# Performance work log

Hardware: AMD Instinct MI355X
Metric: run time of the kernel (lower is better)

Reference implementation:

```python
import jax, jax.numpy as jnp
import numpy as np

N, D, DIN, B, M = 1280000, 128, 2048, 256, 4096
TAU, GAMMA = 0.07, 0.5

def _l2norm(x):
    # F.normalize(p=2, dim=1, eps=1e-12): x / max(||x||, eps)
    n = jnp.sqrt(jnp.sum(x * x, axis=-1, keepdims=True))
    return x / jnp.maximum(n, 1e-12)

def setup_inputs() -> dict:
    key = jax.random.key(0)
    k0, k1, k2, k3, k4, k5 = jax.random.split(key, 6)
    memory_bank = _l2norm(jax.random.normal(k0, (N, D), dtype=jnp.float32))
    outputs = jax.random.normal(k1, (B, DIN), dtype=jnp.float32)
    W = jax.random.normal(k2, (D, DIN), dtype=jnp.float32) * 0.02  # Linear weight (out,in)
    b = jnp.zeros((D,), dtype=jnp.float32)
    indices = jax.random.randint(k3, (B,), 0, N, dtype=jnp.int32)
    random_idxs = jax.random.randint(k4, (B, M), 0, N, dtype=jnp.int32)
    return {"outputs": outputs, "W": W, "b": b, "memory_bank": memory_bank,
            "indices": indices, "random_idxs": random_idxs}

def reference(outputs, W, b, memory_bank, indices, random_idxs):
    batch = outputs.shape[0]
    emb = _l2norm(outputs @ W.T + b)                     # (B, D)
    mb = jax.lax.stop_gradient(memory_bank)              # gathers happen under no_grad
    pos_mem = mb[indices]                                # (B, D) gather
    neg_mem = mb[random_idxs]                            # (B, M, D) gather
    pos = jnp.sum(emb * pos_mem, axis=-1) / TAU          # (B,)
    neg = jnp.einsum('bd,bmd->bm', emb, neg_mem) / TAU   # (B, M)
    # dynamic mode
    log_C_hat = jax.nn.logsumexp(neg, axis=1)            # (B,)
    log_data_prob = pos - jnp.logaddexp(pos, log_C_hat)  # (B,)
    log_noise_prob = log_C_hat[:, None] - jnp.logaddexp(neg, log_C_hat[:, None])  # (B, M)
    data_loss = -jnp.sum(log_data_prob) / batch
    noise_loss = -jnp.sum(log_noise_prob) / batch
    loss = data_loss + noise_loss
    # EMA memory-bank update entries (detached)
    entries = _l2norm(GAMMA * pos_mem + (1.0 - GAMMA) * emb)
    return (loss,
            jax.lax.stop_gradient(entries),
            jax.lax.stop_gradient(data_loss),
            jax.lax.stop_gradient(noise_loss))
```

## Files before the change

### kernel.cpp

```cpp
#include <hip/hip_runtime.h>
#include <math.h>

#define NB 1280000
#define D 128
#define DIN 2048
#define BB 256
#define MM 4096

constexpr float INV_TAU = 1.0f / 0.07f;
constexpr float GAMMA = 0.5f;

__device__ __forceinline__ float softplus_f(float x) {
    return x > 20.0f ? x : log1pf(expf(x));
}

__global__ __launch_bounds__(256) void emb_kernel(
    const float* __restrict__ outputs, const float* __restrict__ W,
    const float* __restrict__ bias, const float* __restrict__ mb,
    const int* __restrict__ indices,
    float* __restrict__ emb, float* __restrict__ pos,
    float* __restrict__ entries)
{
    __shared__ float4 xs4[DIN / 4];
    __shared__ float zbuf[D];
    __shared__ float red[256];
    const int b = blockIdx.x;
    const int t = threadIdx.x;
    const int wave = t >> 6, lane = t & 63;

    const float4* out4 = (const float4*)(outputs + (size_t)b * DIN);
    xs4[t]       = out4[t];
    xs4[t + 256] = out4[t + 256];
    __syncthreads();

    const float4* W4 = (const float4*)W;
    for (int i = 0; i < 32; ++i) {
        int d = i * 4 + wave;
        const float4* wrow = W4 + (size_t)d * (DIN / 4);
        float acc = 0.0f;
        #pragma unroll
        for (int r = 0; r < 8; ++r) {
            float4 wv = wrow[r * 64 + lane];
            float4 xv = xs4[r * 64 + lane];
            acc += wv.x * xv.x + wv.y * xv.y + wv.z * xv.z + wv.w * xv.w;
        }
        #pragma unroll
        for (int s = 32; s > 0; s >>= 1) acc += __shfl_xor(acc, s);
        if (lane == 0) zbuf[d] = acc + bias[d];
    }
    __syncthreads();

    float z = (t < D) ? zbuf[t] : 0.0f;
    red[t] = z * z;
    __syncthreads();
    for (int s = 128; s > 0; s >>= 1) { if (t < s) red[t] += red[t + s]; __syncthreads(); }
    float inv = 1.0f / fmaxf(sqrtf(red[0]), 1e-12f);
    __syncthreads();
    float e = z * inv;
    if (t < D) emb[(size_t)b * D + t] = e;

    int pidx = indices[b];
    float pm = (t < D) ? mb[(size_t)pidx * D + t] : 0.0f;
    red[t] = e * pm;
    __syncthreads();
    for (int s = 128; s > 0; s >>= 1) { if (t < s) red[t] += red[t + s]; __syncthreads(); }
    if (t == 0) pos[b] = red[0] * INV_TAU;
    __syncthreads();

    float en = GAMMA * pm + (1.0f - GAMMA) * e;
    red[t] = en * en;
    __syncthreads();
    for (int s = 128; s > 0; s >>= 1) { if (t < s) red[t] += red[t + s]; __syncthreads(); }
    float inv2 = 1.0f / fmaxf(sqrtf(red[0]), 1e-12f);
    if (t < D) entries[(size_t)b * D + t] = en * inv2;
}

__global__ __launch_bounds__(256) void neg_kernel(
    const float* __restrict__ mb, const int* __restrict__ ridx,
    const float* __restrict__ emb, float* __restrict__ neg,
    float* __restrict__ chunk_max, float* __restrict__ chunk_sum)
{
    __shared__ int idxs[512];
    __shared__ float gmax[8], gsum[8];
    const int blk = blockIdx.x;
    const int b = blk >> 3, c = blk & 7;
    const int m0 = c << 9;
    const int t = threadIdx.x;
    const int g = t >> 5, gl = t & 31;

    idxs[t]       = ridx[(size_t)b * MM + m0 + t];
    idxs[t + 256] = ridx[(size_t)b * MM + m0 + t + 256];
    const float4* emb4 = (const float4*)(emb + (size_t)b * D);
    float4 e4 = emb4[gl];
    __syncthreads();

    const float4* mb4 = (const float4*)mb;
    float* negrow = neg + (size_t)b * MM + m0;
    float mx = -INFINITY, sm = 0.0f;

    for (int it = 0; it < 32; ++it) {
        int r0 = it * 16 + g * 2;
        int i0 = idxs[r0], i1 = idxs[r0 + 1];
        float4 v0 = mb4[(size_t)i0 * 32 + gl];
        float4 v1 = mb4[(size_t)i1 * 32 + gl];
        float p0 = v0.x * e4.x + v0.y * e4.y + v0.z * e4.z + v0.w * e4.w;
        float p1 = v1.x * e4.x + v1.y * e4.y + v1.z * e4.z + v1.w * e4.w;
        #pragma unroll
        for (int s = 16; s > 0; s >>= 1) {
            p0 += __shfl_xor(p0, s);
            p1 += __shfl_xor(p1, s);
        }
        p0 *= INV_TAU; p1 *= INV_TAU;
        if (gl == 0) {
            negrow[r0] = p0; negrow[r0 + 1] = p1;
            float hi = fmaxf(p0, p1), lo = fminf(p0, p1);
            float pairsum = 1.0f + expf(lo - hi);
            if (hi > mx) { sm = sm * expf(mx - hi) + pairsum; mx = hi; }
            else         { sm += pairsum * expf(hi - mx); }
        }
    }
    if (gl == 0) { gmax[g] = mx; gsum[g] = sm; }
    __syncthreads();
    if (t == 0) {
        float Mx = gmax[0];
        for (int i = 1; i < 8; ++i) Mx = fmaxf(Mx, gmax[i]);
        float S = 0.0f;
        for (int i = 0; i < 8; ++i) S += gsum[i] * expf(gmax[i] - Mx);
        chunk_max[blk] = Mx;
        chunk_sum[blk] = S;
    }
}

__global__ __launch_bounds__(256) void logc_kernel(
    const float* __restrict__ chunk_max, const float* __restrict__ chunk_sum,
    const float* __restrict__ pos, float* __restrict__ logC,
    float* __restrict__ data_sum, float* __restrict__ noise_sum)
{
    __shared__ float red[256];
    const int t = threadIdx.x;
    float Mx = -INFINITY;
    for (int i = 0; i < 8; ++i) Mx = fmaxf(Mx, chunk_max[t * 8 + i]);
    float S = 0.0f;
    for (int i = 0; i < 8; ++i) S += chunk_sum[t * 8 + i] * expf(chunk_max[t * 8 + i] - Mx);
    float lc = Mx + logf(S);
    logC[t] = lc;
    red[t] = softplus_f(lc - pos[t]);
    __syncthreads();
    for (int s = 128; s > 0; s >>= 1) { if (t < s) red[t] += red[t + s]; __syncthreads(); }
    if (t == 0) { data_sum[0] = red[0]; noise_sum[0] = 0.0f; }
}

__global__ __launch_bounds__(256) void noise_kernel(
    const float* __restrict__ neg, const float* __restrict__ logC,
    float* __restrict__ noise_sum)
{
    __shared__ float red[256];
    const int t = threadIdx.x;
    size_t i = (size_t)blockIdx.x * 256 + t;
    int b = (int)(i >> 10);
    float lc = logC[b];
    float4 v = ((const float4*)neg)[i];
    float s = softplus_f(v.x - lc) + softplus_f(v.y - lc) +
              softplus_f(v.z - lc) + softplus_f(v.w - lc);
    red[t] = s;
    __syncthreads();
    for (int st = 128; st > 0; st >>= 1) { if (t < st) red[t] += red[t + st]; __syncthreads(); }
    if (t == 0) atomicAdd(noise_sum, red[0]);
}

__global__ void final_kernel(const float* __restrict__ data_sum,
                             const float* __restrict__ noise_sum,
                             float* __restrict__ out)
{
    float dl = data_sum[0] / (float)BB;
    float nl = noise_sum[0] / (float)BB;
    out[0] = dl + nl;
    out[1 + BB * D] = dl;
    out[2 + BB * D] = nl;
}

extern "C" void kernel_launch(void* const* d_in, const int* in_sizes, int n_in,
                              void* d_out, int out_size, void* d_ws, size_t ws_size,
                              hipStream_t stream) {
    const float* outputs = (const float*)d_in[0];
    const float* W       = (const float*)d_in[1];
    const float* bias    = (const float*)d_in[2];
    const float* mb      = (const float*)d_in[3];
    const int*   indices = (const int*)d_in[4];
    const int*   ridx    = (const int*)d_in[5];

    float* out = (float*)d_out;
    float* ws  = (float*)d_ws;

    float* emb       = ws;
    float* pos       = emb + BB * D;
    float* chunk_max = pos + BB;
    float* chunk_sum = chunk_max + BB * 8;
    float* logC      = chunk_sum + BB * 8;
    float* data_sum  = logC + BB;
    float* noise_sum = data_sum + 1;
    float* neg       = ws + 37380;

    float* entries = out + 1;

    emb_kernel<<<BB, 256, 0, stream>>>(outputs, W, bias, mb, indices, emb, pos, entries);
    neg_kernel<<<BB * 8, 256, 0, stream>>>(mb, ridx, emb, neg, chunk_max, chunk_sum);
    logc_kernel<<<1, 256, 0, stream>>>(chunk_max, chunk_sum, pos, logC, data_sum, noise_sum);
    noise_kernel<<<BB * MM / 4 / 256, 256, 0, stream>>>(neg, logC, noise_sum);
    final_kernel<<<1, 1, 0, stream>>>(data_sum, noise_sum, out);
}
```

Baseline: 867.7 us.

## Batch eight gathered rows per group and parallelize chunk logsumexp in neg_kernel

Each 32-lane group now issues eight independent memory-bank row gathers before reducing, instead of two per iteration. This raises memory-level parallelism on the random gather. Dot products are staged in shared memory, so the stores to neg become coalesced block-wide writes. The serial per-lane online softmax is replaced by block-wide max and sum reductions. Costs are more registers per thread and extra shared memory and barriers.

```diff
diff --git a/kernel.cpp b/kernel.cpp
--- a/kernel.cpp
+++ b/kernel.cpp
@@ -81,53 +81,59 @@
     float* __restrict__ chunk_max, float* __restrict__ chunk_sum)
 {
     __shared__ int idxs[512];
-    __shared__ float gmax[8], gsum[8];
+    __shared__ float pvals[512];
+    __shared__ float wm[4], wsum[4];
     const int blk = blockIdx.x;
     const int b = blk >> 3, c = blk & 7;
     const int m0 = c << 9;
     const int t = threadIdx.x;
     const int g = t >> 5, gl = t & 31;
+    const int wave = t >> 6, lane = t & 63;
 
     idxs[t]       = ridx[(size_t)b * MM + m0 + t];
-    idxs[t + 256] = ridx[(size_t)b * MM + m0 + t + 256];
-    const float4* emb4 = (const float4*)(emb + (size_t)b * D);
-    float4 e4 = emb4[gl];
+    idxs[t + 256] = ridx[(size_t)b * MM + m0 + 256 + t];
+    float4 e4 = ((const float4*)(emb + (size_t)b * D))[gl];
     __syncthreads();
 
     const float4* mb4 = (const float4*)mb;
+
+    for (int it = 0; it < 8; ++it) {
+        const int r0 = it * 64 + g * 8;
+        float4 v[8];
+        #pragma unroll
+        for (int j = 0; j < 8; ++j)
+            v[j] = mb4[(size_t)idxs[r0 + j] * 32 + gl];
+        float myp = 0.0f;
+        #pragma unroll
+        for (int j = 0; j < 8; ++j) {
+            float p = v[j].x * e4.x + v[j].y * e4.y + v[j].z * e4.z + v[j].w * e4.w;
+            #pragma unroll
+            for (int s = 16; s > 0; s >>= 1) p += __shfl_xor(p, s);
+            if (gl == j) myp = p;
+        }
+        if (gl < 8) pvals[r0 + gl] = myp * INV_TAU;
+    }
+    __syncthreads();
+
+    float v0 = pvals[t], v1 = pvals[t + 256];
     float* negrow = neg + (size_t)b * MM + m0;
-    float mx = -INFINITY, sm = 0.0f;
-
-    for (int it = 0; it < 32; ++it) {
-        int r0 = it * 16 + g * 2;
-        int i0 = idxs[r0], i1 = idxs[r0 + 1];
-        float4 v0 = mb4[(size_t)i0 * 32 + gl];
-        float4 v1 = mb4[(size_t)i1 * 32 + gl];
-        float p0 = v0.x * e4.x + v0.y * e4.y + v0.z * e4.z + v0.w * e4.w;
-        float p1 = v1.x * e4.x + v1.y * e4.y + v1.z * e4.z + v1.w * e4.w;
-        #pragma unroll
-        for (int s = 16; s > 0; s >>= 1) {
-            p0 += __shfl_xor(p0, s);
-            p1 += __shfl_xor(p1, s);
-        }
-        p0 *= INV_TAU; p1 *= INV_TAU;
-        if (gl == 0) {
-            negrow[r0] = p0; negrow[r0 + 1] = p1;
-            float hi = fmaxf(p0, p1), lo = fminf(p0, p1);
-            float pairsum = 1.0f + expf(lo - hi);
-            if (hi > mx) { sm = sm * expf(mx - hi) + pairsum; mx = hi; }
-            else         { sm += pairsum * expf(hi - mx); }
-        }
-    }
-    if (gl == 0) { gmax[g] = mx; gsum[g] = sm; }
+    negrow[t]       = v0;
+    negrow[t + 256] = v1;
+
+    float m = fmaxf(v0, v1);
+    #pragma unroll
+    for (int s = 32; s > 0; s >>= 1) m = fmaxf(m, __shfl_xor(m, s));
+    if (lane == 0) wm[wave] = m;
+    __syncthreads();
+    float Mx = fmaxf(fmaxf(wm[0], wm[1]), fmaxf(wm[2], wm[3]));
+    float s2 = expf(v0 - Mx) + expf(v1 - Mx);
+    #pragma unroll
+    for (int s = 32; s > 0; s >>= 1) s2 += __shfl_xor(s2, s);
+    if (lane == 0) wsum[wave] = s2;
     __syncthreads();
     if (t == 0) {
-        float Mx = gmax[0];
-        for (int i = 1; i < 8; ++i) Mx = fmaxf(Mx, gmax[i]);
-        float S = 0.0f;
-        for (int i = 0; i < 8; ++i) S += gsum[i] * expf(gmax[i] - Mx);
         chunk_max[blk] = Mx;
-        chunk_sum[blk] = S;
+        chunk_sum[blk] = wsum[0] + wsum[1] + wsum[2] + wsum[3];
     }
 }
 
```

Result: no change. 860.4 us (-0.8%).
